# Optimization experiments

Hardware: AMD Instinct MI355X
Metric: run time of the kernel (lower is better)

## Reference

```python
import jax, jax.numpy as jnp
import numpy as np

B = 16384
D = 1024
NG = 64
H = 2  # num_heads = len(conv_kernel_sizes)


def setup_inputs() -> dict:
    key = jax.random.key(0)
    ks = jax.random.split(key, 12)
    s = 0.02
    return {
        "x": jax.random.normal(ks[0], (B, D), jnp.float32),
        "group_labels": jax.random.randint(ks[1], (B,), 0, NG, dtype=jnp.int32),
        "num_groups": NG,
        "conv_w2": jax.random.normal(ks[2], (2,), jnp.float32) * s,
        "conv_b2": jax.random.normal(ks[3], (), jnp.float32) * s,
        "conv_w4": jax.random.normal(ks[4], (4,), jnp.float32) * s,
        "conv_b4": jax.random.normal(ks[5], (), jnp.float32) * s,
        "intra_in_w": jax.random.normal(ks[6], (3 * D, D), jnp.float32) * s,
        "intra_in_b": jnp.zeros((3 * D,), jnp.float32),
        "intra_out_w": jax.random.normal(ks[7], (D, D), jnp.float32) * s,
        "intra_out_b": jnp.zeros((D,), jnp.float32),
        "inter_in_w": jax.random.normal(ks[8], (3 * D, D), jnp.float32) * s,
        "inter_in_b": jnp.zeros((3 * D,), jnp.float32),
        "inter_out_w": jax.random.normal(ks[9], (D, D), jnp.float32) * s,
        "inter_out_b": jnp.zeros((D,), jnp.float32),
        "lin_w": jax.random.normal(ks[10], (D, D), jnp.float32) * s,
        "lin_b": jnp.zeros((D,), jnp.float32),
    }


def _seg_conv(x_s, l_s, w, b):
    """Per-group Conv2d(1,1,(k,1),padding=(k//2,0)) along the group-sorted axis,
    with zero padding at group boundaries and output trimmed to group size.
    out[i] = sum_j w[j] * x[i + j - k//2] if same group else 0."""
    n = x_s.shape[0]
    k = w.shape[0]
    pad = k // 2
    xp = jnp.pad(x_s, ((pad, pad), (0, 0)))
    lp = jnp.pad(l_s, (pad, pad), constant_values=-1)
    out = jnp.zeros_like(x_s)
    for j in range(k):  # k <= 4, static
        m = (lp[j:j + n] == l_s)[:, None]
        out = out + w[j] * jnp.where(m, xp[j:j + n], 0.0)
    return out + b


def _mha_self(xs, in_w, in_b, out_w, out_b, h):
    """torch nn.MultiheadAttention self-attention, seq-first xs: [S, N, D]."""
    S, N, Dm = xs.shape
    dh = Dm // h
    qkv = jnp.einsum('snd,ed->sne', xs, in_w) + in_b
    q, k, v = jnp.split(qkv, 3, axis=-1)
    q = q.reshape(S, N, h, dh)
    k = k.reshape(S, N, h, dh)
    v = v.reshape(S, N, h, dh)
    scores = jnp.einsum('qnhd,knhd->nhqk', q, k) / np.float32(np.sqrt(dh))
    a = jax.nn.softmax(scores, axis=-1)
    o = jnp.einsum('nhqk,knhd->qnhd', a, v).reshape(S, N, Dm)
    return jnp.einsum('snd,ed->sne', o, out_w) + out_b


def reference(x, group_labels, num_groups, conv_w2, conv_b2, conv_w4, conv_b4,
              intra_in_w, intra_in_b, intra_out_w, intra_out_b,
              inter_in_w, inter_in_b, inter_out_w, inter_out_b, lin_w, lin_b):
    n, d = x.shape
    labels = group_labels.astype(jnp.int32)
    perm = jnp.argsort(labels)  # stable: preserves original order within groups
    x_s = x[perm]
    l_s = labels[perm]

    # per-group convs -> [2, N, D] token stack (seq-first for MHA)
    t2 = _seg_conv(x_s, l_s, conv_w2, conv_b2)
    t4 = _seg_conv(x_s, l_s, conv_w4, conv_b4)
    tok = jnp.stack([t2, t4], axis=0)

    # intra attention over the 2 conv tokens per position, mean, then Linear
    intra = _mha_self(tok, intra_in_w, intra_in_b, intra_out_w, intra_out_b, H).mean(axis=0)
    lin_out = intra @ lin_w.T + lin_b  # [N, D]

    # inter-group: seq-len-1 attention over FIRST row of each other group ==
    # out_proj(v_proj(first_row)); mean over the other present groups.
    counts = jax.ops.segment_sum(jnp.ones((n,), jnp.int32), labels, num_segments=num_groups)
    present = counts > 0
    first_idx = jax.ops.segment_min(jnp.arange(n), labels, num_segments=num_groups)
    first_rows = x[jnp.where(present, first_idx, 0)]  # [NG, D]
    Wv = inter_in_w[2 * d:]
    bv = inter_in_b[2 * d:]
    f = (first_rows @ Wv.T + bv) @ inter_out_w.T + inter_out_b  # [NG, D]
    f = jnp.where(present[:, None], f, 0.0)
    n_present = jnp.sum(present.astype(jnp.int32))
    denom = jnp.maximum(n_present - 1, 1).astype(x.dtype)
    inter_mean = (jnp.sum(f, axis=0)[None, :] - f) / denom
    inter_mean = inter_mean * (n_present > 1).astype(x.dtype)

    out_s = lin_out + inter_mean[l_s]
    return jnp.zeros_like(x).at[perm].set(out_s)
```

## Files before the change

kernel.cpp:

```cpp
#include <hip/hip_runtime.h>
#include <hip/hip_bf16.h>

#define B_N 16384
#define D_DIM 1024
#define NGRP 64
#define NCHUNK 64
#define CHUNK 256

typedef __attribute__((ext_vector_type(8))) short short8;
typedef __attribute__((ext_vector_type(8))) unsigned short ushort8;
typedef __attribute__((ext_vector_type(4))) unsigned short ushort4v;
typedef __attribute__((ext_vector_type(4))) float floatx4;

__device__ __forceinline__ float bf2f(unsigned short h) {
    union { unsigned u; float f; } c; c.u = ((unsigned)h) << 16; return c.f;
}
__device__ __forceinline__ unsigned short f2bf(float f) {
    union { float f; unsigned u; } c; c.f = f;
    unsigned r = c.u + 0x7FFFu + ((c.u >> 16) & 1u);
    return (unsigned short)(r >> 16);
}

__device__ __forceinline__ void gload_lds16(const void* g, void* l) {
    __builtin_amdgcn_global_load_lds(
        (const __attribute__((address_space(1))) unsigned int*)g,
        (__attribute__((address_space(3))) unsigned int*)l, 16, 0, 0);
}

__global__ __launch_bounds__(256) void k_hist(const int* __restrict__ labels,
                                              int* __restrict__ hist) {
    __shared__ int lh[NGRP];
    int t = threadIdx.x, c = blockIdx.x;
    if (t < NGRP) lh[t] = 0;
    __syncthreads();
    int lab = labels[c * CHUNK + t];
    atomicAdd(&lh[lab], 1);
    __syncthreads();
    if (t < NGRP) hist[c * NGRP + t] = lh[t];
}

__global__ void k_scan(int* __restrict__ hist, int* __restrict__ gstart,
                       int* __restrict__ counts, float* __restrict__ scal) {
    __shared__ int cnt[NGRP];
    __shared__ int st[NGRP + 1];
    int g = threadIdx.x;
    int run = 0;
    for (int c = 0; c < NCHUNK; c++) {
        int v = hist[c * NGRP + g];
        hist[c * NGRP + g] = run;
        run += v;
    }
    cnt[g] = run;
    counts[g] = run;
    __syncthreads();
    if (g == 0) {
        int s = 0, np = 0;
        for (int i = 0; i < NGRP; i++) { st[i] = s; s += cnt[i]; np += (cnt[i] > 0); }
        st[NGRP] = s;
        scal[0] = (np > 1) ? 1.0f / (float)(np - 1) : 0.0f;
    }
    __syncthreads();
    gstart[g] = st[g];
    if (g == 0) gstart[NGRP] = st[NGRP];
    for (int c = 0; c < NCHUNK; c++) hist[c * NGRP + g] += st[g];
}

__global__ __launch_bounds__(256) void k_scatter(const int* __restrict__ labels,
                                                 const int* __restrict__ hist,
                                                 int* __restrict__ perm,
                                                 int* __restrict__ ls) {
    __shared__ int lab[CHUNK];
    int c = blockIdx.x, t = threadIdx.x;
    int i = c * CHUNK + t;
    int L = labels[i];
    lab[t] = L;
    __syncthreads();
    int rank = 0;
    for (int j = 0; j < t; j++) rank += (lab[j] == L);
    int pos = hist[c * NGRP + L] + rank;
    perm[pos] = i;
    ls[pos] = L;
}

__global__ __launch_bounds__(256) void k_conv(const float* __restrict__ x,
                                              const int* __restrict__ perm,
                                              const int* __restrict__ ls,
                                              const float* __restrict__ w2, const float* __restrict__ b2,
                                              const float* __restrict__ w4, const float* __restrict__ b4,
                                              unsigned short* __restrict__ tok, int c0, int Bc) {
    const int il = blockIdx.x;
    const int i = c0 + il;
    const int li = ls[i];
    const int p0 = perm[i];
    const int pm1 = (i >= 1 && ls[i - 1] == li) ? perm[i - 1] : -1;
    const int pm2 = (i >= 2 && ls[i - 2] == li) ? perm[i - 2] : -1;
    const int pp1 = (i + 1 < B_N && ls[i + 1] == li) ? perm[i + 1] : -1;
    const int c = threadIdx.x * 4;
    floatx4 z = (floatx4)0.0f;
    floatx4 x0 = *(const floatx4*)(x + (size_t)p0 * D_DIM + c);
    floatx4 xm1 = (pm1 >= 0) ? *(const floatx4*)(x + (size_t)pm1 * D_DIM + c) : z;
    floatx4 xm2 = (pm2 >= 0) ? *(const floatx4*)(x + (size_t)pm2 * D_DIM + c) : z;
    floatx4 xp1 = (pp1 >= 0) ? *(const floatx4*)(x + (size_t)pp1 * D_DIM + c) : z;
    const float w20 = w2[0], w21 = w2[1], cb2 = b2[0];
    const float w40 = w4[0], w41 = w4[1], w42 = w4[2], w43 = w4[3], cb4 = b4[0];
    ushort4v o2, o4;
#pragma unroll
    for (int j = 0; j < 4; j++) {
        float t2 = w20 * xm1[j] + w21 * x0[j] + cb2;
        float t4 = w40 * xm2[j] + w41 * xm1[j] + w42 * x0[j] + w43 * xp1[j] + cb4;
        o2[j] = f2bf(t2);
        o4[j] = f2bf(t4);
    }
    *(ushort4v*)(tok + (size_t)il * D_DIM + c) = o2;
    *(ushort4v*)(tok + (size_t)(Bc + il) * D_DIM + c) = o4;
}

__global__ __launch_bounds__(256) void k_cast4(const float* __restrict__ src,
                                               unsigned short* __restrict__ dst, int n4) {
    int i = blockIdx.x * 256 + threadIdx.x;
    if (i < n4) {
        floatx4 v = *(const floatx4*)(src + (size_t)i * 4);
        ushort4v o;
#pragma unroll
        for (int j = 0; j < 4; j++) o[j] = f2bf(v[j]);
        *(ushort4v*)(dst + (size_t)i * 4) = o;
    }
}

__global__ __launch_bounds__(256) void k_tcast(const float* __restrict__ src,
                                               unsigned short* __restrict__ dst) {
    __shared__ float tile[32][33];
    int bx = blockIdx.x * 32, by = blockIdx.y * 32;
    int tx = threadIdx.x & 31, ty = threadIdx.x >> 5;
    for (int r = ty; r < 32; r += 8) tile[r][tx] = src[(size_t)(by + r) * D_DIM + bx + tx];
    __syncthreads();
    for (int r = ty; r < 32; r += 8) dst[(size_t)(bx + r) * D_DIM + by + tx] = f2bf(tile[tx][r]);
}

__global__ __launch_bounds__(256) void k_biasc(const float* __restrict__ lin_w,
                                               const float* __restrict__ lin_b,
                                               const float* __restrict__ ob,
                                               float* __restrict__ biasc) {
    int n = blockIdx.x * 256 + threadIdx.x;
    float s = lin_b[n];
    const float* wr = lin_w + (size_t)n * D_DIM;
    for (int t = 0; t < D_DIM; t++) s += ob[t] * wr[t];
    biasc[n] = s;
}

__global__ __launch_bounds__(256) void k_u(const float* __restrict__ x,
                                           const int* __restrict__ perm,
                                           const int* __restrict__ gstart,
                                           const int* __restrict__ counts,
                                           const float* __restrict__ Wfull,
                                           const float* __restrict__ bfull,
                                           float* __restrict__ u) {
    const int g = blockIdx.y;
    const int n = blockIdx.x * 256 + threadIdx.x;
    __shared__ __align__(16) float xr[D_DIM];
    const int cnt = counts[g];
    const int row = (cnt > 0) ? perm[gstart[g]] : 0;
    for (int k = threadIdx.x; k < D_DIM; k += 256) xr[k] = x[(size_t)row * D_DIM + k];
    __syncthreads();
    const floatx4* wr4 = (const floatx4*)(Wfull + (size_t)(2 * D_DIM + n) * D_DIM);
    const floatx4* xr4 = (const floatx4*)xr;
    float s = bfull[2 * D_DIM + n];
    for (int k4 = 0; k4 < D_DIM / 4; k4++) {
        floatx4 a = xr4[k4], b = wr4[k4];
        s += a[0] * b[0] + a[1] * b[1] + a[2] * b[2] + a[3] * b[3];
    }
    u[g * D_DIM + n] = s;
}

__global__ __launch_bounds__(256) void k_f(const float* __restrict__ u,
                                           const int* __restrict__ counts,
                                           const float* __restrict__ W,
                                           const float* __restrict__ b,
                                           float* __restrict__ f) {
    const int g = blockIdx.y;
    const int n = blockIdx.x * 256 + threadIdx.x;
    __shared__ __align__(16) float ur[D_DIM];
    const int cnt = counts[g];
    for (int k = threadIdx.x; k < D_DIM; k += 256) ur[k] = u[g * D_DIM + k];
    __syncthreads();
    const floatx4* wr4 = (const floatx4*)(W + (size_t)n * D_DIM);
    const floatx4* ur4 = (const floatx4*)ur;
    float s = b[n];
    for (int k4 = 0; k4 < D_DIM / 4; k4++) {
        floatx4 a = ur4[k4], w = wr4[k4];
        s += a[0] * w[0] + a[1] * w[1] + a[2] * w[2] + a[3] * w[3];
    }
    f[g * D_DIM + n] = (cnt > 0) ? s : 0.0f;
}

__global__ __launch_bounds__(256) void k_imean(const float* __restrict__ f,
                                               const float* __restrict__ scal,
                                               float* __restrict__ im) {
    int c = blockIdx.x * 256 + threadIdx.x;
    float s = 0.0f;
    for (int g = 0; g < NGRP; g++) s += f[g * D_DIM + c];
    float fl = scal[0];
    for (int g = 0; g < NGRP; g++) im[g * D_DIM + c] = (s - f[g * D_DIM + c]) * fl;
}

template <int MODE>
__global__ __launch_bounds__(256)
void gemm_bt(const unsigned short* __restrict__ A,
             const unsigned short* __restrict__ W,
             int M, int N, int K,
             const float* __restrict__ bias,
             unsigned short* __restrict__ outb,
             float* __restrict__ outf,
             const int* __restrict__ perm,
             const int* __restrict__ ls,
             const float* __restrict__ imean) {
    __shared__ __align__(16) unsigned short sA[128 * 64];
    __shared__ __align__(16) unsigned short sB[128 * 64];
    const int t = threadIdx.x;
    const int lane = t & 63, wv = t >> 6;
    const int m0 = blockIdx.y * 128, n0 = blockIdx.x * 128;
    const int wm = (wv & 1) * 64, wn = (wv >> 1) * 64;
    const int l15 = lane & 15, quad = lane >> 4;
    const int sw = l15 & 7;

    floatx4 acc[4][4];
#pragma unroll
    for (int i = 0; i < 4; i++)
#pragma unroll
        for (int j = 0; j < 4; j++) acc[i][j] = (floatx4)0.0f;

    for (int k0 = 0; k0 < K; k0 += 64) {
#pragma unroll
        for (int r = 0; r < 4; r++) {
            const int chunk = r * 256 + wv * 64;
            const int idx = chunk + lane;
            const int row = idx >> 3;
            const int kb = (idx & 7) ^ (row & 7);
            gload_lds16(A + (size_t)(m0 + row) * K + k0 + kb * 8, &sA[chunk * 8]);
            gload_lds16(W + (size_t)(n0 + row) * K + k0 + kb * 8, &sB[chunk * 8]);
        }
        __syncthreads();
#pragma unroll
        for (int kk = 0; kk < 64; kk += 32) {
            const int kc = kk >> 3;
            short8 av[4], bv[4];
#pragma unroll
            for (int mt = 0; mt < 4; mt++)
                av[mt] = *(const short8*)&sA[(wm + mt * 16 + l15) * 64 +
                                             (((kc + quad) ^ sw) << 3)];
#pragma unroll
            for (int nt = 0; nt < 4; nt++)
                bv[nt] = *(const short8*)&sB[(wn + nt * 16 + l15) * 64 +
                                             (((kc + quad) ^ sw) << 3)];
#pragma unroll
            for (int mt = 0; mt < 4; mt++)
#pragma unroll
                for (int nt = 0; nt < 4; nt++)
                    acc[mt][nt] = __builtin_amdgcn_mfma_f32_16x16x32_bf16(
                        av[mt], bv[nt], acc[mt][nt], 0, 0, 0);
        }
        __syncthreads();
    }

    if (MODE == 0 || MODE == 1) {
#pragma unroll
        for (int nt = 0; nt < 4; nt++) {
            const int gc = n0 + wn + nt * 16 + l15;
            const float bb = (MODE == 0) ? bias[gc] : 0.0f;
#pragma unroll
            for (int mt = 0; mt < 4; mt++) {
                const int gr = m0 + wm + mt * 16 + quad * 4;
#pragma unroll
                for (int r = 0; r < 4; r++)
                    outb[(size_t)(gr + r) * N + gc] = f2bf(acc[mt][nt][r] + bb);
            }
        }
    } else {
        float bb[4];
        int gc4[4];
#pragma unroll
        for (int nt = 0; nt < 4; nt++) {
            gc4[nt] = n0 + wn + nt * 16 + l15;
            bb[nt] = bias[gc4[nt]];
        }
#pragma unroll
        for (int mt = 0; mt < 4; mt++) {
#pragma unroll
            for (int r = 0; r < 4; r++) {
                const int i = m0 + wm + mt * 16 + quad * 4 + r;
                const int orow = perm[i];
                const int lg = ls[i];
#pragma unroll
                for (int nt = 0; nt < 4; nt++)
                    outf[(size_t)orow * N + gc4[nt]] =
                        acc[mt][nt][r] + bb[nt] + imean[lg * D_DIM + gc4[nt]];
            }
        }
    }
}

__global__ __launch_bounds__(256) void k_attn(const unsigned short* __restrict__ qkv,
                                              unsigned short* __restrict__ om,
                                              int c0, int Bc) {
    const int t = threadIdx.x;
    const int lane = t & 63, wv = t >> 6;
    const int bl = blockIdx.x * 4 + wv;
    const size_t r0 = (size_t)bl * 3072;
    const size_t r1 = (size_t)(Bc + bl) * 3072;
    float c0w[2], c1w[2];
#pragma unroll
    for (int h = 0; h < 2; h++) {
        const int off = h * 512 + lane * 8;
        short8 q0 = *(const short8*)(qkv + r0 + off);
        short8 q1 = *(const short8*)(qkv + r1 + off);
        short8 k0 = *(const short8*)(qkv + r0 + 1024 + off);
        short8 k1 = *(const short8*)(qkv + r1 + 1024 + off);
        float s00 = 0, s01 = 0, s10 = 0, s11 = 0;
#pragma unroll
        for (int j = 0; j < 8; j++) {
            float q0f = bf2f((unsigned short)q0[j]), q1f = bf2f((unsigned short)q1[j]);
            float k0f = bf2f((unsigned short)k0[j]), k1f = bf2f((unsigned short)k1[j]);
            s00 += q0f * k0f; s01 += q0f * k1f; s10 += q1f * k0f; s11 += q1f * k1f;
        }
#pragma unroll
        for (int d = 32; d > 0; d >>= 1) {
            s00 += __shfl_xor(s00, d, 64);
            s01 += __shfl_xor(s01, d, 64);
            s10 += __shfl_xor(s10, d, 64);
            s11 += __shfl_xor(s11, d, 64);
        }
        const float sc = 0.044194173824159216f;
        s00 *= sc; s01 *= sc; s10 *= sc; s11 *= sc;
        float m0 = fmaxf(s00, s01), e00 = __expf(s00 - m0), e01 = __expf(s01 - m0);
        float w01 = e01 / (e00 + e01), w00 = 1.0f - w01;
        float m1 = fmaxf(s10, s11), e10 = __expf(s10 - m1), e11 = __expf(s11 - m1);
        float w11 = e11 / (e10 + e11), w10 = 1.0f - w11;
        c0w[h] = 0.5f * (w00 + w10);
        c1w[h] = 0.5f * (w01 + w11);
    }
#pragma unroll
    for (int h = 0; h < 2; h++) {
        const int off = h * 512 + lane * 8;
        short8 v0 = *(const short8*)(qkv + r0 + 2048 + off);
        short8 v1 = *(const short8*)(qkv + r1 + 2048 + off);
        ushort8 o;
#pragma unroll
        for (int j = 0; j < 8; j++) {
            float val = c0w[h] * bf2f((unsigned short)v0[j]) + c1w[h] * bf2f((unsigned short)v1[j]);
            o[j] = f2bf(val);
        }
        *(ushort8*)(om + (size_t)(c0 + bl) * D_DIM + off) = o;
    }
}

extern "C" void kernel_launch(void* const* d_in, const int* in_sizes, int n_in,
                              void* d_out, int out_size, void* d_ws, size_t ws_size,
                              hipStream_t stream) {
    const float* x = (const float*)d_in[0];
    const int* labels = (const int*)d_in[1];
    const float* conv_w2 = (const float*)d_in[3];
    const float* conv_b2 = (const float*)d_in[4];
    const float* conv_w4 = (const float*)d_in[5];
    const float* conv_b4 = (const float*)d_in[6];
    const float* intra_in_w = (const float*)d_in[7];
    const float* intra_in_b = (const float*)d_in[8];
    const float* intra_out_w = (const float*)d_in[9];
    const float* intra_out_b = (const float*)d_in[10];
    const float* inter_in_w = (const float*)d_in[11];
    const float* inter_in_b = (const float*)d_in[12];
    const float* inter_out_w = (const float*)d_in[13];
    const float* inter_out_b = (const float*)d_in[14];
    const float* lin_w = (const float*)d_in[15];
    const float* lin_b = (const float*)d_in[16];
    float* out = (float*)d_out;

    char* p = (char*)d_ws;
    auto alloc = [&](size_t bytes) -> void* {
        void* r = (void*)p;
        p += (bytes + 255) & ~(size_t)255;
        return r;
    };
    int* perm = (int*)alloc(B_N * 4);
    int* lss = (int*)alloc(B_N * 4);
    int* hist = (int*)alloc(NCHUNK * NGRP * 4);
    int* gstart = (int*)alloc((NGRP + 1) * 4);
    int* counts = (int*)alloc(NGRP * 4);
    float* scal = (float*)alloc(4);
    unsigned short* om = (unsigned short*)alloc((size_t)B_N * D_DIM * 2);
    unsigned short* W1b = (unsigned short*)alloc((size_t)3 * D_DIM * D_DIM * 2);
    unsigned short* linwb = (unsigned short*)alloc((size_t)D_DIM * D_DIM * 2);
    unsigned short* WoT = (unsigned short*)alloc((size_t)D_DIM * D_DIM * 2);
    unsigned short* Wc = (unsigned short*)alloc((size_t)D_DIM * D_DIM * 2);
    float* u = (float*)alloc((size_t)NGRP * D_DIM * 4);
    float* fbuf = (float*)alloc((size_t)NGRP * D_DIM * 4);
    float* imean = (float*)alloc((size_t)NGRP * D_DIM * 4);
    float* biasc = (float*)alloc(D_DIM * 4);

    size_t used = (size_t)(p - (char*)d_ws);
    size_t remain = (ws_size > used) ? (ws_size - used) : 0;
    int Bc = 512;
    const int cand[6] = {16384, 8192, 4096, 2048, 1024, 512};
    for (int ci = 0; ci < 6; ci++) {
        if ((size_t)16384 * cand[ci] + 8192 <= remain) { Bc = cand[ci]; break; }
    }
    unsigned short* tokc = (unsigned short*)alloc((size_t)2 * Bc * D_DIM * 2);
    unsigned short* qkvc = (unsigned short*)alloc((size_t)2 * Bc * 3 * D_DIM * 2);

    k_hist<<<NCHUNK, CHUNK, 0, stream>>>(labels, hist);
    k_scan<<<1, NGRP, 0, stream>>>(hist, gstart, counts, scal);
    k_scatter<<<NCHUNK, CHUNK, 0, stream>>>(labels, hist, perm, lss);
    k_cast4<<<(3 * D_DIM * D_DIM / 4 + 255) / 256, 256, 0, stream>>>(intra_in_w, W1b,
                                                                     3 * D_DIM * D_DIM / 4);
    k_cast4<<<(D_DIM * D_DIM / 4 + 255) / 256, 256, 0, stream>>>(lin_w, linwb,
                                                                 D_DIM * D_DIM / 4);
    k_tcast<<<dim3(32, 32), 256, 0, stream>>>(intra_out_w, WoT);
    gemm_bt<1><<<dim3(8, 8), 256, 0, stream>>>(linwb, WoT, 1024, 1024, 1024, nullptr, Wc,
                                               nullptr, nullptr, nullptr, nullptr);
    k_biasc<<<4, 256, 0, stream>>>(lin_w, lin_b, intra_out_b, biasc);
    k_u<<<dim3(4, NGRP), 256, 0, stream>>>(x, perm, gstart, counts, inter_in_w, inter_in_b, u);
    k_f<<<dim3(4, NGRP), 256, 0, stream>>>(u, counts, inter_out_w, inter_out_b, fbuf);
    k_imean<<<4, 256, 0, stream>>>(fbuf, scal, imean);
    const int nchunks = B_N / Bc;
    for (int c = 0; c < nchunks; c++) {
        const int c0 = c * Bc;
        k_conv<<<Bc, 256, 0, stream>>>(x, perm, lss, conv_w2, conv_b2, conv_w4, conv_b4,
                                       tokc, c0, Bc);
        gemm_bt<0><<<dim3(24, 2 * Bc / 128), 256, 0, stream>>>(
            tokc, W1b, 2 * Bc, 3 * D_DIM, D_DIM, intra_in_b, qkvc, nullptr, nullptr,
            nullptr, nullptr);
        k_attn<<<Bc / 4, 256, 0, stream>>>(qkvc, om, c0, Bc);
    }
    gemm_bt<2><<<dim3(8, 128), 256, 0, stream>>>(om, Wc, B_N, D_DIM, D_DIM, biasc, nullptr,
                                                 out, perm, lss, imean);
}
```

Measured before the change: 668.1 us.

## Apply attention weights before V projection to shrink the intra QKV GEMM

Uses linearity of the V projection: the two attention-weighted conv tokens are combined first (per head), then projected with Wv. The QKV GEMM now computes only Q and K (2048 columns) on 2*Bc rows, and V becomes a Bc-row GEMM on the pre-mixed tokens, which drops about a third of that FLOP cost. The change also fuses the weight-cast kernels and the bias-combine kernel into existing launches and adds an XCD-aware block remap to the GEMM. In exchange it adds extra kernels per chunk (score, z-prep) and a bf16 round-trip of the mixed tokens, which may change rounding slightly.

```diff
diff --git a/kernel.cpp b/kernel.cpp
--- a/kernel.cpp
+++ b/kernel.cpp
@@ -115,37 +115,36 @@
     *(ushort4v*)(tok + (size_t)(Bc + il) * D_DIM + c) = o4;
 }
 
-__global__ __launch_bounds__(256) void k_cast4(const float* __restrict__ src,
-                                               unsigned short* __restrict__ dst, int n4) {
-    int i = blockIdx.x * 256 + threadIdx.x;
-    if (i < n4) {
-        floatx4 v = *(const floatx4*)(src + (size_t)i * 4);
+__global__ __launch_bounds__(256) void k_prep(const float* __restrict__ intra_in_w,
+                                              const float* __restrict__ lin_w,
+                                              const float* __restrict__ intra_out_w,
+                                              unsigned short* __restrict__ W1b,
+                                              unsigned short* __restrict__ linwb,
+                                              unsigned short* __restrict__ WoT) {
+    __shared__ float tile[32][33];
+    const int bx = blockIdx.x;
+    if (bx < 4096) {
+        int i = bx * 256 + threadIdx.x;
+        const float* src;
+        unsigned short* dst;
+        int j;
+        if (i < 786432) { src = intra_in_w; dst = W1b; j = i; }
+        else { src = lin_w; dst = linwb; j = i - 786432; }
+        floatx4 v = *(const floatx4*)(src + (size_t)j * 4);
         ushort4v o;
 #pragma unroll
-        for (int j = 0; j < 4; j++) o[j] = f2bf(v[j]);
-        *(ushort4v*)(dst + (size_t)i * 4) = o;
-    }
-}
-
-__global__ __launch_bounds__(256) void k_tcast(const float* __restrict__ src,
-                                               unsigned short* __restrict__ dst) {
-    __shared__ float tile[32][33];
-    int bx = blockIdx.x * 32, by = blockIdx.y * 32;
-    int tx = threadIdx.x & 31, ty = threadIdx.x >> 5;
-    for (int r = ty; r < 32; r += 8) tile[r][tx] = src[(size_t)(by + r) * D_DIM + bx + tx];
-    __syncthreads();
-    for (int r = ty; r < 32; r += 8) dst[(size_t)(bx + r) * D_DIM + by + tx] = f2bf(tile[tx][r]);
-}
-
-__global__ __launch_bounds__(256) void k_biasc(const float* __restrict__ lin_w,
-                                               const float* __restrict__ lin_b,
-                                               const float* __restrict__ ob,
-                                               float* __restrict__ biasc) {
-    int n = blockIdx.x * 256 + threadIdx.x;
-    float s = lin_b[n];
-    const float* wr = lin_w + (size_t)n * D_DIM;
-    for (int t = 0; t < D_DIM; t++) s += ob[t] * wr[t];
-    biasc[n] = s;
+        for (int q = 0; q < 4; q++) o[q] = f2bf(v[q]);
+        *(ushort4v*)(dst + (size_t)j * 4) = o;
+    } else {
+        const int tb = bx - 4096;
+        const int bX = (tb & 31) * 32, bY = (tb >> 5) * 32;
+        const int tx = threadIdx.x & 31, ty = threadIdx.x >> 5;
+        for (int r = ty; r < 32; r += 8)
+            tile[r][tx] = intra_out_w[(size_t)(bY + r) * D_DIM + bX + tx];
+        __syncthreads();
+        for (int r = ty; r < 32; r += 8)
+            WoT[(size_t)(bX + r) * D_DIM + bY + tx] = f2bf(tile[tx][r]);
+    }
 }
 
 __global__ __launch_bounds__(256) void k_u(const float* __restrict__ x,
@@ -154,22 +153,34 @@
                                            const int* __restrict__ counts,
                                            const float* __restrict__ Wfull,
                                            const float* __restrict__ bfull,
-                                           float* __restrict__ u) {
+                                           float* __restrict__ u,
+                                           const float* __restrict__ lin_w,
+                                           const float* __restrict__ lin_b,
+                                           const float* __restrict__ ob,
+                                           float* __restrict__ biasc) {
     const int g = blockIdx.y;
     const int n = blockIdx.x * 256 + threadIdx.x;
     __shared__ __align__(16) float xr[D_DIM];
-    const int cnt = counts[g];
-    const int row = (cnt > 0) ? perm[gstart[g]] : 0;
-    for (int k = threadIdx.x; k < D_DIM; k += 256) xr[k] = x[(size_t)row * D_DIM + k];
-    __syncthreads();
-    const floatx4* wr4 = (const floatx4*)(Wfull + (size_t)(2 * D_DIM + n) * D_DIM);
+    const bool isb = (g == NGRP);
+    int row = 0;
+    if (!isb) {
+        const int cnt = counts[g];
+        row = (cnt > 0) ? perm[gstart[g]] : 0;
+    }
+    for (int k = threadIdx.x; k < D_DIM; k += 256)
+        xr[k] = isb ? ob[k] : x[(size_t)row * D_DIM + k];
+    __syncthreads();
+    const float* wrow = isb ? (lin_w + (size_t)n * D_DIM)
+                            : (Wfull + (size_t)(2 * D_DIM + n) * D_DIM);
+    const floatx4* wr4 = (const floatx4*)wrow;
     const floatx4* xr4 = (const floatx4*)xr;
-    float s = bfull[2 * D_DIM + n];
+    float s = isb ? lin_b[n] : bfull[2 * D_DIM + n];
     for (int k4 = 0; k4 < D_DIM / 4; k4++) {
         floatx4 a = xr4[k4], b = wr4[k4];
         s += a[0] * b[0] + a[1] * b[1] + a[2] * b[2] + a[3] * b[3];
     }
-    u[g * D_DIM + n] = s;
+    if (isb) biasc[n] = s;
+    else u[g * D_DIM + n] = s;
 }
 
 __global__ __launch_bounds__(256) void k_f(const float* __restrict__ u,
@@ -213,12 +224,23 @@
              float* __restrict__ outf,
              const int* __restrict__ perm,
              const int* __restrict__ ls,
-             const float* __restrict__ imean) {
+             const float* __restrict__ imean,
+             int mhstride, int ldc, int rowoff) {
     __shared__ __align__(16) unsigned short sA[128 * 64];
     __shared__ __align__(16) unsigned short sB[128 * 64];
     const int t = threadIdx.x;
     const int lane = t & 63, wv = t >> 6;
-    const int m0 = blockIdx.y * 128, n0 = blockIdx.x * 128;
+    int bx = blockIdx.x, by = blockIdx.y;
+    const int nX = gridDim.x, nY = gridDim.y;
+    if ((nY & 7) == 0) {
+        const int bid = by * nX + bx;
+        const int xcd = bid & 7, j = bid >> 3;
+        const int stripe = nY >> 3;
+        by = xcd * stripe + j / nX;
+        bx = j % nX;
+    }
+    const int m0 = by * 128, n0 = bx * 128;
+    if (MODE == 3) A += (size_t)(n0 >> 9) * (size_t)mhstride;
     const int wm = (wv & 1) * 64, wn = (wv >> 1) * 64;
     const int l15 = lane & 15, quad = lane >> 4;
     const int sw = l15 & 7;
@@ -262,17 +284,19 @@
         __syncthreads();
     }
 
-    if (MODE == 0 || MODE == 1) {
+    if (MODE != 2) {
+        const int ld = (MODE == 3) ? ldc : N;
+        const int rb = (MODE == 3) ? rowoff : 0;
 #pragma unroll
         for (int nt = 0; nt < 4; nt++) {
             const int gc = n0 + wn + nt * 16 + l15;
-            const float bb = (MODE == 0) ? bias[gc] : 0.0f;
+            const float bb = (MODE == 1) ? 0.0f : bias[gc];
 #pragma unroll
             for (int mt = 0; mt < 4; mt++) {
                 const int gr = m0 + wm + mt * 16 + quad * 4;
 #pragma unroll
                 for (int r = 0; r < 4; r++)
-                    outb[(size_t)(gr + r) * N + gc] = f2bf(acc[mt][nt][r] + bb);
+                    outb[(size_t)(rb + gr + r) * ld + gc] = f2bf(acc[mt][nt][r] + bb);
             }
         }
     } else {
@@ -299,58 +323,69 @@
     }
 }
 
-__global__ __launch_bounds__(256) void k_attn(const unsigned short* __restrict__ qkv,
-                                              unsigned short* __restrict__ om,
-                                              int c0, int Bc) {
+__global__ __launch_bounds__(256) void k_score(const unsigned short* __restrict__ qk,
+                                               floatx4* __restrict__ gam, int Bc) {
     const int t = threadIdx.x;
     const int lane = t & 63, wv = t >> 6;
     const int bl = blockIdx.x * 4 + wv;
-    const size_t r0 = (size_t)bl * 3072;
-    const size_t r1 = (size_t)(Bc + bl) * 3072;
-    float c0w[2], c1w[2];
+    const unsigned short* r2 = qk + (size_t)bl * 2048;
+    const unsigned short* r4 = qk + (size_t)(Bc + bl) * 2048;
+    float cw[4];
 #pragma unroll
     for (int h = 0; h < 2; h++) {
         const int off = h * 512 + lane * 8;
-        short8 q0 = *(const short8*)(qkv + r0 + off);
-        short8 q1 = *(const short8*)(qkv + r1 + off);
-        short8 k0 = *(const short8*)(qkv + r0 + 1024 + off);
-        short8 k1 = *(const short8*)(qkv + r1 + 1024 + off);
-        float s00 = 0, s01 = 0, s10 = 0, s11 = 0;
+        short8 q2 = *(const short8*)(r2 + off);
+        short8 q4 = *(const short8*)(r4 + off);
+        short8 k2 = *(const short8*)(r2 + 1024 + off);
+        short8 k4 = *(const short8*)(r4 + 1024 + off);
+        float s22 = 0, s24 = 0, s42 = 0, s44 = 0;
 #pragma unroll
         for (int j = 0; j < 8; j++) {
-            float q0f = bf2f((unsigned short)q0[j]), q1f = bf2f((unsigned short)q1[j]);
-            float k0f = bf2f((unsigned short)k0[j]), k1f = bf2f((unsigned short)k1[j]);
-            s00 += q0f * k0f; s01 += q0f * k1f; s10 += q1f * k0f; s11 += q1f * k1f;
+            float q2f = bf2f((unsigned short)q2[j]), q4f = bf2f((unsigned short)q4[j]);
+            float k2f = bf2f((unsigned short)k2[j]), k4f = bf2f((unsigned short)k4[j]);
+            s22 += q2f * k2f; s24 += q2f * k4f; s42 += q4f * k2f; s44 += q4f * k4f;
         }
 #pragma unroll
         for (int d = 32; d > 0; d >>= 1) {
-            s00 += __shfl_xor(s00, d, 64);
-            s01 += __shfl_xor(s01, d, 64);
-            s10 += __shfl_xor(s10, d, 64);
-            s11 += __shfl_xor(s11, d, 64);
+            s22 += __shfl_xor(s22, d, 64);
+            s24 += __shfl_xor(s24, d, 64);
+            s42 += __shfl_xor(s42, d, 64);
+            s44 += __shfl_xor(s44, d, 64);
         }
         const float sc = 0.044194173824159216f;
-        s00 *= sc; s01 *= sc; s10 *= sc; s11 *= sc;
-        float m0 = fmaxf(s00, s01), e00 = __expf(s00 - m0), e01 = __expf(s01 - m0);
-        float w01 = e01 / (e00 + e01), w00 = 1.0f - w01;
-        float m1 = fmaxf(s10, s11), e10 = __expf(s10 - m1), e11 = __expf(s11 - m1);
-        float w11 = e11 / (e10 + e11), w10 = 1.0f - w11;
-        c0w[h] = 0.5f * (w00 + w10);
-        c1w[h] = 0.5f * (w01 + w11);
-    }
-#pragma unroll
-    for (int h = 0; h < 2; h++) {
-        const int off = h * 512 + lane * 8;
-        short8 v0 = *(const short8*)(qkv + r0 + 2048 + off);
-        short8 v1 = *(const short8*)(qkv + r1 + 2048 + off);
-        ushort8 o;
-#pragma unroll
-        for (int j = 0; j < 8; j++) {
-            float val = c0w[h] * bf2f((unsigned short)v0[j]) + c1w[h] * bf2f((unsigned short)v1[j]);
-            o[j] = f2bf(val);
-        }
-        *(ushort8*)(om + (size_t)(c0 + bl) * D_DIM + off) = o;
-    }
+        s22 *= sc; s24 *= sc; s42 *= sc; s44 *= sc;
+        float m0 = fmaxf(s22, s24), e22 = __expf(s22 - m0), e24 = __expf(s24 - m0);
+        float w24 = e24 / (e22 + e24), w22 = 1.0f - w24;
+        float m1 = fmaxf(s42, s44), e42 = __expf(s42 - m1), e44 = __expf(s44 - m1);
+        float w44 = e44 / (e42 + e44), w42 = 1.0f - w44;
+        cw[h * 2 + 0] = 0.5f * (w22 + w42);
+        cw[h * 2 + 1] = 0.5f * (w24 + w44);
+    }
+    if (lane == 0) {
+        floatx4 g;
+        g[0] = cw[0]; g[1] = cw[1]; g[2] = cw[2]; g[3] = cw[3];
+        gam[bl] = g;
+    }
+}
+
+__global__ __launch_bounds__(256) void k_zprep(const unsigned short* __restrict__ tok,
+                                               const floatx4* __restrict__ gam,
+                                               unsigned short* __restrict__ z, int Bc) {
+    const int idx = blockIdx.x * 256 + threadIdx.x;
+    const int bl = idx >> 7;
+    const int seg = (idx & 127) * 8;
+    floatx4 g = gam[bl];
+    short8 a = *(const short8*)(tok + (size_t)bl * D_DIM + seg);
+    short8 b = *(const short8*)(tok + (size_t)(Bc + bl) * D_DIM + seg);
+    ushort8 z1, z2;
+#pragma unroll
+    for (int j = 0; j < 8; j++) {
+        float af = bf2f((unsigned short)a[j]), bf = bf2f((unsigned short)b[j]);
+        z1[j] = f2bf(g[0] * af + g[1] * bf);
+        z2[j] = f2bf(g[2] * af + g[3] * bf);
+    }
+    *(ushort8*)(z + (size_t)bl * D_DIM + seg) = z1;
+    *(ushort8*)(z + (size_t)(Bc + bl) * D_DIM + seg) = z2;
 }
 
 extern "C" void kernel_launch(void* const* d_in, const int* in_sizes, int n_in,
@@ -401,23 +436,22 @@
     int Bc = 512;
     const int cand[6] = {16384, 8192, 4096, 2048, 1024, 512};
     for (int ci = 0; ci < 6; ci++) {
-        if ((size_t)16384 * cand[ci] + 8192 <= remain) { Bc = cand[ci]; break; }
+        if ((size_t)16400 * cand[ci] + 8192 <= remain) { Bc = cand[ci]; break; }
     }
     unsigned short* tokc = (unsigned short*)alloc((size_t)2 * Bc * D_DIM * 2);
-    unsigned short* qkvc = (unsigned short*)alloc((size_t)2 * Bc * 3 * D_DIM * 2);
+    unsigned short* qkc = (unsigned short*)alloc((size_t)2 * Bc * 2 * D_DIM * 2);
+    unsigned short* zc = (unsigned short*)alloc((size_t)2 * Bc * D_DIM * 2);
+    floatx4* gam = (floatx4*)alloc((size_t)Bc * 16);
 
     k_hist<<<NCHUNK, CHUNK, 0, stream>>>(labels, hist);
     k_scan<<<1, NGRP, 0, stream>>>(hist, gstart, counts, scal);
     k_scatter<<<NCHUNK, CHUNK, 0, stream>>>(labels, hist, perm, lss);
-    k_cast4<<<(3 * D_DIM * D_DIM / 4 + 255) / 256, 256, 0, stream>>>(intra_in_w, W1b,
-                                                                     3 * D_DIM * D_DIM / 4);
-    k_cast4<<<(D_DIM * D_DIM / 4 + 255) / 256, 256, 0, stream>>>(lin_w, linwb,
-                                                                 D_DIM * D_DIM / 4);
-    k_tcast<<<dim3(32, 32), 256, 0, stream>>>(intra_out_w, WoT);
+    k_prep<<<4096 + 1024, 256, 0, stream>>>(intra_in_w, lin_w, intra_out_w, W1b, linwb, WoT);
     gemm_bt<1><<<dim3(8, 8), 256, 0, stream>>>(linwb, WoT, 1024, 1024, 1024, nullptr, Wc,
-                                               nullptr, nullptr, nullptr, nullptr);
-    k_biasc<<<4, 256, 0, stream>>>(lin_w, lin_b, intra_out_b, biasc);
-    k_u<<<dim3(4, NGRP), 256, 0, stream>>>(x, perm, gstart, counts, inter_in_w, inter_in_b, u);
+                                               nullptr, nullptr, nullptr, nullptr, 0, 0, 0);
+    k_u<<<dim3(4, NGRP + 1), 256, 0, stream>>>(x, perm, gstart, counts, inter_in_w,
+                                               inter_in_b, u, lin_w, lin_b, intra_out_b,
+                                               biasc);
     k_f<<<dim3(4, NGRP), 256, 0, stream>>>(u, counts, inter_out_w, inter_out_b, fbuf);
     k_imean<<<4, 256, 0, stream>>>(fbuf, scal, imean);
     const int nchunks = B_N / Bc;
@@ -425,11 +459,16 @@
         const int c0 = c * Bc;
         k_conv<<<Bc, 256, 0, stream>>>(x, perm, lss, conv_w2, conv_b2, conv_w4, conv_b4,
                                        tokc, c0, Bc);
-        gemm_bt<0><<<dim3(24, 2 * Bc / 128), 256, 0, stream>>>(
-            tokc, W1b, 2 * Bc, 3 * D_DIM, D_DIM, intra_in_b, qkvc, nullptr, nullptr,
-            nullptr, nullptr);
-        k_attn<<<Bc / 4, 256, 0, stream>>>(qkvc, om, c0, Bc);
+        gemm_bt<0><<<dim3(16, 2 * Bc / 128), 256, 0, stream>>>(
+            tokc, W1b, 2 * Bc, 2 * D_DIM, D_DIM, intra_in_b, qkc, nullptr, nullptr,
+            nullptr, nullptr, 0, 0, 0);
+        k_score<<<Bc / 4, 256, 0, stream>>>(qkc, gam, Bc);
+        k_zprep<<<Bc / 2, 256, 0, stream>>>(tokc, gam, zc, Bc);
+        gemm_bt<3><<<dim3(8, Bc / 128), 256, 0, stream>>>(
+            zc, W1b + (size_t)2 * D_DIM * D_DIM, Bc, D_DIM, D_DIM,
+            intra_in_b + 2 * D_DIM, om, nullptr, nullptr, nullptr, nullptr,
+            Bc * D_DIM, D_DIM, c0);
     }
     gemm_bt<2><<<dim3(8, 128), 256, 0, stream>>>(om, Wc, B_N, D_DIM, D_DIM, biasc, nullptr,
-                                                 out, perm, lss, imean);
-}
+                                                 out, perm, lss, imean, 0, 0, 0);
+}
```

After: 649.2 us. 2.8% less time.
